# Kernel tuning notes

Hardware: AMD Instinct MI355X
Metric: run time of the kernel (lower is better)

Reference implementation:

```python
import jax, jax.numpy as jnp
import numpy as np

N, M, K = 131072, 32, 16
EPS64 = 2.220446049250313e-16  # np.finfo(np.float64).eps, as in the original


def setup_inputs() -> dict:
    key = jax.random.key(0)
    k1, k2, k3, k4, k5 = jax.random.split(key, 5)
    X = jax.random.normal(k1, (N, M), dtype=jnp.float32)
    Wk0 = jax.random.normal(k2, (K,), dtype=jnp.float32)
    W = jax.random.normal(k3, (M, K, K), dtype=jnp.float32)
    mu = jax.random.uniform(k4, (K, K), minval=-4.0, maxval=4.0, dtype=jnp.float32)
    sigma = 0.5 + 0.5 * jax.random.uniform(k5, (K, K), dtype=jnp.float32)
    return {"X": X, "Wk0": Wk0, "W": W, "mu": mu, "sigma": sigma}


def reference(X, Wk0, W, mu, sigma):
    # Softmax-normalized TT weights (original: softmax(Wk0), softmax(W, axis=1))
    z = jax.nn.softmax(Wk0)          # (K,)
    Wn = jax.nn.softmax(W, axis=1)   # (M, K, K)
    inv_norm = 1.0 / (sigma * jnp.sqrt(2.0 * jnp.pi))  # (K, K) Gaussian normalizer

    def step(v, inp):
        # v: (N, K) running left-product z @ resT_0 @ ... @ resT_{i-1}
        x_i, w_i = inp               # x_i: (N,), w_i: (K, K)
        d = (x_i[:, None, None] - mu) / sigma          # (N, K, K)
        B = jnp.exp(-0.5 * d * d) * inv_norm           # Normal(mu, sigma).prob(x)
        res = w_i[None, :, :] * B                      # res[n,a,b] == original res[a,b,n]
        # original: products = products @ res.T, so v_new[n,b] = sum_a v[n,a] * res[n,b,a]
        v_new = jnp.einsum('na,nba->nb', v, res)
        return v_new, None

    v0 = jnp.broadcast_to(z, (X.shape[0], z.shape[0]))   # z @ identity start
    v_final, _ = jax.lax.scan(step, v0, (X.T, Wn))       # scan over M steps
    likelihoods = jnp.sum(v_final, axis=1)               # sum(z @ products, axis=1)
    return jnp.log(likelihoods + EPS64)
```

## Files before the change

### kernel.cpp

```cpp
#include <hip/hip_runtime.h>
#include <cmath>


#define TT_N 131072
#define TT_M 32

typedef float v2f __attribute__((ext_vector_type(2)));
typedef float v4f __attribute__((ext_vector_type(4)));

#define WS_Z 0
#define WS_P 16
#define WS_Q (16 + 256)
#define WS_R (16 + 512)
#define TBL_FLOATS (512 + 8192)

__global__ __launch_bounds__(512) void tt_prep(const float* __restrict__ Wk0,
                                               const float* __restrict__ W,
                                               const float* __restrict__ mu,
                                               const float* __restrict__ sigma,
                                               float* __restrict__ ws) {
    const int t = threadIdx.x;
    const float LOG2E = 1.4426950408889634f;
    const float SCALE = 8388608.0f;
    const float BIAS  = 126.94242f;
    float* z  = ws + WS_Z;
    float* PP = ws + WS_P;
    float* QQ = ws + WS_Q;
    float* RT = ws + WS_R;

    if (t < 16) {
        float mx = -1e30f;
        for (int i = 0; i < 16; ++i) mx = fmaxf(mx, Wk0[i]);
        float se = 0.f;
        for (int i = 0; i < 16; ++i) se += __expf(Wk0[i] - mx);
        z[t] = __expf(Wk0[t] - mx) / se;
    }

    if (t < 256) {
        const int a = t >> 4, b = t & 15;
        float s  = sigma[b * 16 + a];
        float mm = mu[b * 16 + a];
        float c2 = 0.72134752044448f / (s * s);
        PP[a * 16 + b] = -c2 * SCALE;
        QQ[a * 16 + b] = 2.0f * c2 * mm * SCALE;
    }

    const int m = t >> 4;
    const int a = t & 15;
    const float* Wc = W + m * 256 + a;
    float mx = -1e30f;
    #pragma unroll
    for (int b = 0; b < 16; ++b) mx = fmaxf(mx, Wc[b * 16]);
    float se = 0.f;
    #pragma unroll
    for (int b = 0; b < 16; ++b) se += __expf(Wc[b * 16] - mx);
    float lse = __log2f(se);
    #pragma unroll
    for (int b = 0; b < 16; ++b) {
        float s     = sigma[b * 16 + a];
        float mm    = mu[b * 16 + a];
        float inv_s = 1.0f / s;
        float c2    = 0.72134752044448f / (s * s);
        float lw    = (Wc[b * 16] - mx) * LOG2E - lse;
        float R = lw + __log2f(inv_s * 0.3989422804014327f) - c2 * mm * mm;
        RT[m * 256 + a * 16 + b] = (R + BIAS) * SCALE;
    }
}

static __device__ __forceinline__ v2f shfl_xor_v2f(v2f x, int mask) {
    v2f r;
    r.x = __shfl_xor(x.x, mask, 64);
    r.y = __shfl_xor(x.y, mask, 64);
    return r;
}

static __device__ __forceinline__ v2f fast_exp2_pair(v2f s) {
    s = __builtin_elementwise_max(s, (v2f){0.f, 0.f});
    v2f e;
    e.x = __int_as_float((int)s.x);
    e.y = __int_as_float((int)s.y);
    return e;
}

__global__ __launch_bounds__(512) void tt_main(const float* __restrict__ X,
                                               const float* __restrict__ ws,
                                               float* __restrict__ out) {
    __shared__ float lds[TBL_FLOATS];
    {
        const v4f* src = (const v4f*)(ws + WS_P);
        v4f* dst = (v4f*)lds;
        for (int i = threadIdx.x; i < TBL_FLOATS / 4; i += 512) dst[i] = src[i];
    }
    __syncthreads();

    const int tid  = blockIdx.x * 512 + threadIdx.x;
    const int n    = tid >> 2;
    const int g    = tid & 3;
    const int boff = g << 2;

    const float* zp = ws + WS_Z;
    v2f v[8];
    #pragma unroll
    for (int p = 0; p < 8; ++p) v[p] = (v2f){zp[2 * p], zp[2 * p + 1]};

    const float* xp = X + (size_t)n * TT_M;
    float S = 1.f;
    float xn = xp[0];

    #pragma unroll 1
    for (int m = 0; m < TT_M; ++m) {
        const float xm = xn;
        xn = xp[(m + 1 < TT_M) ? m + 1 : m];
        const float xq = xm * xm;
        const v2f xx  = {xm, xm};
        const v2f xx2 = {xq, xq};

        int lo = 0;
        asm volatile("" : "+v"(lo));
        const float* Pm = lds + lo;
        const float* Qm = lds + 256 + lo;
        const float* Rm = lds + 512 + m * 256;

        v2f a0, a1;

        #pragma unroll
        for (int a = 0; a < 16; ++a) {
            const float vas = (a & 1) ? v[a >> 1].y : v[a >> 1].x;
            const v2f va2 = {vas, vas};
            const int base = a * 16 + boff;
            v4f P4 = *(const v4f*)(Pm + base);
            v4f Q4 = *(const v4f*)(Qm + base);
            v4f R4 = *(const v4f*)(Rm + base);
            v2f t0 = __builtin_elementwise_fma(Q4.xy, xx, R4.xy);
            v2f s0 = __builtin_elementwise_fma(P4.xy, xx2, t0);
            v2f t1 = __builtin_elementwise_fma(Q4.zw, xx, R4.zw);
            v2f s1 = __builtin_elementwise_fma(P4.zw, xx2, t1);
            v2f e0 = fast_exp2_pair(s0);
            v2f e1 = fast_exp2_pair(s1);
            if (a == 0) { a0 = va2 * e0; a1 = va2 * e1; }
            else {
                a0 = __builtin_elementwise_fma(va2, e0, a0);
                a1 = __builtin_elementwise_fma(va2, e1, a1);
            }
        }

        const bool hi1 = (g & 1) != 0;
        const bool hi2 = (g & 2) != 0;
        v2f r0 = shfl_xor_v2f(a0, 1), r1 = shfl_xor_v2f(a1, 1);
        v2f u0 = hi1 ? r0 : a0;
        v2f u1 = hi1 ? r1 : a1;
        v2f u2 = hi1 ? a0 : r0;
        v2f u3 = hi1 ? a1 : r1;
        v2f w0 = shfl_xor_v2f(u0, 2), w1 = shfl_xor_v2f(u1, 2);
        v2f w2 = shfl_xor_v2f(u2, 2), w3 = shfl_xor_v2f(u3, 2);
        v[0] = hi2 ? w0 : u0;  v[1] = hi2 ? w1 : u1;
        v[2] = hi2 ? w2 : u2;  v[3] = hi2 ? w3 : u3;
        v[4] = hi2 ? u0 : w0;  v[5] = hi2 ? u1 : w1;
        v[6] = hi2 ? u2 : w2;  v[7] = hi2 ? u3 : w3;

        v2f q0 = (v[0] + v[1]) + (v[2] + v[3]);
        v2f q1 = (v[4] + v[5]) + (v[6] + v[7]);
        v2f q  = q0 + q1;
        S = q.x + q.y;
        if (__all(S < 5e-17f)) break;
    }

    if (g == 0) out[n] = logf(S + 2.2204460492503131e-16f);
}

extern "C" void kernel_launch(void* const* d_in, const int* in_sizes, int n_in,
                              void* d_out, int out_size, void* d_ws, size_t ws_size,
                              hipStream_t stream) {
    const float* X     = (const float*)d_in[0];
    const float* Wk0   = (const float*)d_in[1];
    const float* W     = (const float*)d_in[2];
    const float* mu    = (const float*)d_in[3];
    const float* sigma = (const float*)d_in[4];
    float* out = (float*)d_out;
    float* ws  = (float*)d_ws;

    tt_prep<<<1, 512, 0, stream>>>(Wk0, W, mu, sigma, ws);
    tt_main<<<(TT_N * 4) / 512, 512, 0, stream>>>(X, ws, out);
}
```

Measured before the change: 99.28 us.

## Read coefficient tables from global cache and use DPP for quad exchanges

Removes the per-block copy of the P/Q/R tables into shared memory and the barrier, loading coefficients directly from the workspace through the cache hierarchy. Replaces the xor shuffles (which go through the LDS crossbar) with DPP quad-permute moves for the intra-quad transpose. This cuts LDS traffic and block startup cost, but global-cache loads have higher latency than LDS reads inside the hot loop.

```diff
diff --git a/kernel.cpp b/kernel.cpp
--- a/kernel.cpp
+++ b/kernel.cpp
@@ -12,7 +12,6 @@
 #define WS_P 16
 #define WS_Q (16 + 256)
 #define WS_R (16 + 512)
-#define TBL_FLOATS (512 + 8192)
 
 __global__ __launch_bounds__(512) void tt_prep(const float* __restrict__ Wk0,
                                                const float* __restrict__ W,
@@ -67,10 +66,13 @@
     }
 }
 
-static __device__ __forceinline__ v2f shfl_xor_v2f(v2f x, int mask) {
+template <int CTRL>
+static __device__ __forceinline__ v2f dpp_v2f(v2f x) {
     v2f r;
-    r.x = __shfl_xor(x.x, mask, 64);
-    r.y = __shfl_xor(x.y, mask, 64);
+    r.x = __int_as_float(
+        __builtin_amdgcn_mov_dpp(__float_as_int(x.x), CTRL, 0xF, 0xF, 1));
+    r.y = __int_as_float(
+        __builtin_amdgcn_mov_dpp(__float_as_int(x.y), CTRL, 0xF, 0xF, 1));
     return r;
 }
 
@@ -85,14 +87,6 @@
 __global__ __launch_bounds__(512) void tt_main(const float* __restrict__ X,
                                                const float* __restrict__ ws,
                                                float* __restrict__ out) {
-    __shared__ float lds[TBL_FLOATS];
-    {
-        const v4f* src = (const v4f*)(ws + WS_P);
-        v4f* dst = (v4f*)lds;
-        for (int i = threadIdx.x; i < TBL_FLOATS / 4; i += 512) dst[i] = src[i];
-    }
-    __syncthreads();
-
     const int tid  = blockIdx.x * 512 + threadIdx.x;
     const int n    = tid >> 2;
     const int g    = tid & 3;
@@ -117,9 +111,9 @@
 
         int lo = 0;
         asm volatile("" : "+v"(lo));
-        const float* Pm = lds + lo;
-        const float* Qm = lds + 256 + lo;
-        const float* Rm = lds + 512 + m * 256;
+        const float* Pm = ws + WS_P + boff + lo;
+        const float* Qm = ws + WS_Q + boff + lo;
+        const float* Rm = ws + WS_R + m * 256 + boff + lo;
 
         v2f a0, a1;
 
@@ -127,10 +121,9 @@
         for (int a = 0; a < 16; ++a) {
             const float vas = (a & 1) ? v[a >> 1].y : v[a >> 1].x;
             const v2f va2 = {vas, vas};
-            const int base = a * 16 + boff;
-            v4f P4 = *(const v4f*)(Pm + base);
-            v4f Q4 = *(const v4f*)(Qm + base);
-            v4f R4 = *(const v4f*)(Rm + base);
+            v4f P4 = *(const v4f*)(Pm + a * 16);
+            v4f Q4 = *(const v4f*)(Qm + a * 16);
+            v4f R4 = *(const v4f*)(Rm + a * 16);
             v2f t0 = __builtin_elementwise_fma(Q4.xy, xx, R4.xy);
             v2f s0 = __builtin_elementwise_fma(P4.xy, xx2, t0);
             v2f t1 = __builtin_elementwise_fma(Q4.zw, xx, R4.zw);
@@ -146,13 +139,13 @@
 
         const bool hi1 = (g & 1) != 0;
         const bool hi2 = (g & 2) != 0;
-        v2f r0 = shfl_xor_v2f(a0, 1), r1 = shfl_xor_v2f(a1, 1);
+        v2f r0 = dpp_v2f<0xB1>(a0), r1 = dpp_v2f<0xB1>(a1);
         v2f u0 = hi1 ? r0 : a0;
         v2f u1 = hi1 ? r1 : a1;
         v2f u2 = hi1 ? a0 : r0;
         v2f u3 = hi1 ? a1 : r1;
-        v2f w0 = shfl_xor_v2f(u0, 2), w1 = shfl_xor_v2f(u1, 2);
-        v2f w2 = shfl_xor_v2f(u2, 2), w3 = shfl_xor_v2f(u3, 2);
+        v2f w0 = dpp_v2f<0x4E>(u0), w1 = dpp_v2f<0x4E>(u1);
+        v2f w2 = dpp_v2f<0x4E>(u2), w3 = dpp_v2f<0x4E>(u3);
         v[0] = hi2 ? w0 : u0;  v[1] = hi2 ? w1 : u1;
         v[2] = hi2 ? w2 : u2;  v[3] = hi2 ? w3 : u3;
         v[4] = hi2 ? u0 : w0;  v[5] = hi2 ? u1 : w1;
```

New measurement: 220.6 us. 122% more time.
